# Kernel optimization log

Measured on AMD Instinct MI355X. Metric: run time of the kernel, lower is better.

## Reference

```python
import jax, jax.numpy as jnp
import numpy as np

N = 100_000        # nodes
E = 1_600_000      # edges (avg degree 16)
IN_DIM = 128
OUT_DIM = 128
EPS = 1e-5         # gnn.BatchNorm default eps


def setup_inputs() -> dict:
    key = jax.random.key(0)
    ks = jax.random.split(key, 4)
    x = jax.random.normal(ks[0], (N, IN_DIM), dtype=jnp.float32)
    edge_index = jax.random.randint(ks[1], (2, E), 0, N, dtype=jnp.int32)
    # ChebConv weights: one [indim,outdim] Linear (no bias) per hop k=0..2, plus shared bias
    W = jax.random.normal(ks[2], (3, IN_DIM, OUT_DIM), dtype=jnp.float32) / np.float32(np.sqrt(IN_DIM))
    bias = jnp.zeros((OUT_DIM,), jnp.float32)
    a_prelu = jnp.float32(0.25)           # nn.PReLU default init
    gamma = jnp.ones((OUT_DIM,), jnp.float32)
    beta = jnp.zeros((OUT_DIM,), jnp.float32)
    return dict(x=x, edge_index=edge_index, W=W, bias=bias,
                a_prelu=a_prelu, gamma=gamma, beta=beta)


def reference(x, edge_index, W, bias, a_prelu, gamma, beta):
    src, dst = edge_index[0], edge_index[1]
    n = x.shape[0]
    # --- scaled Laplacian L_hat = 2L/lambda_max - I, sym norm, lambda_max=2 ---
    # diagonal of L_hat is exactly 0 (1 from L's identity minus the -1 self-loop),
    # so only off-diagonal entries -d_i^{-1/2} d_j^{-1/2} remain.
    deg = jax.ops.segment_sum(jnp.ones_like(src, dtype=x.dtype), src, num_segments=n)
    dinv = jnp.where(deg > 0, jax.lax.rsqrt(deg), jnp.zeros_like(deg))
    norm = -(dinv[src] * dinv[dst])  # [E]

    def lhat(v):  # sparse matvec: out[i] = sum_{(j->i)} norm * v[j]
        return jax.ops.segment_sum(v[src] * norm[:, None], dst, num_segments=n)

    # --- Chebyshev recursion, K=3 ---
    tx0 = x
    tx1 = lhat(x)
    tx2 = 2.0 * lhat(tx1) - tx0
    out = tx0 @ W[0] + tx1 @ W[1] + tx2 @ W[2] + bias

    # --- PReLU (single shared parameter) ---
    out = jnp.where(out >= 0, out, a_prelu * out)

    # --- BatchNorm over nodes (training-mode batch stats, biased var) ---
    mean = out.mean(axis=0)
    var = out.var(axis=0)
    out = (out - mean) * jax.lax.rsqrt(var + EPS) * gamma + beta
    return out
```

## Files before the change

kernel.cpp:

```cpp
#include <hip/hip_runtime.h>
#include <cstdint>
#include <cstddef>

#define EPS 1e-5f
#define CAP 64
#define CHUNK 4096
#define NBMAX 256

typedef __attribute__((ext_vector_type(8))) short short8;
typedef __attribute__((ext_vector_type(4))) float f32x4;

static __device__ __forceinline__ short f2bf(float f) {
    uint32_t u = __float_as_uint(f);
    u += 0x7FFFu + ((u >> 16) & 1u);
    return (short)(u >> 16);
}
static __device__ __forceinline__ float bf2f(short s) {
    return __uint_as_float(((uint32_t)(uint16_t)s) << 16);
}

__global__ __launch_bounds__(256) void k_prep(
        const int* __restrict__ src, const int* __restrict__ dst, int E,
        const float* __restrict__ x, const float* __restrict__ W,
        int* __restrict__ bcur, int2* __restrict__ breg,
        int* __restrict__ sbcur, int* __restrict__ sbreg,
        int REGCAP, int NBK, short* __restrict__ xbf, short* __restrict__ WT,
        int BB, int SB, int TB, int t8) {
    int b = blockIdx.x;
    int t = threadIdx.x;
    __shared__ int hist[NBMAX], sexc[NBMAX], cur[NBMAX], gb[NBMAX];
    __shared__ int wsum[4];
    __shared__ int2 stage[CHUNK];
    if (b < BB) {
        int e0 = b * CHUNK;
        int2 ed[16];
        #pragma unroll
        for (int k = 0; k < 16; ++k) {
            int i = e0 + k * 256 + t;
            ed[k].x = (i < E) ? src[i] : 0;
            ed[k].y = (i < E) ? dst[i] : -1;
        }
        hist[t] = 0;
        __syncthreads();
        #pragma unroll
        for (int k = 0; k < 16; ++k)
            if (ed[k].y >= 0) atomicAdd(&hist[ed[k].y >> 9], 1);
        __syncthreads();
        int lane = t & 63, wv = t >> 6;
        int val = hist[t];
        int incl = val;
        #pragma unroll
        for (int off = 1; off < 64; off <<= 1) {
            int v = __shfl_up(incl, off);
            if (lane >= off) incl += v;
        }
        if (lane == 63) wsum[wv] = incl;
        __syncthreads();
        int bw = 0;
        for (int r = 0; r < wv; ++r) bw += wsum[r];
        int excl = bw + incl - val;
        sexc[t] = excl;
        cur[t] = excl;
        gb[t] = (val > 0 && t < NBK) ? atomicAdd(&bcur[t], val) : 0;
        __syncthreads();
        #pragma unroll
        for (int k = 0; k < 16; ++k) {
            if (ed[k].y >= 0) {
                int p = atomicAdd(&cur[ed[k].y >> 9], 1);
                stage[p] = ed[k];
            }
        }
        __syncthreads();
        int C = E - e0; if (C > CHUNK) C = CHUNK;
        for (int idx = t; idx < C; idx += 256) {
            int2 e = stage[idx];
            int bb = e.y >> 9;
            int pos = gb[bb] + (idx - sexc[bb]);
            if (pos < REGCAP) breg[(size_t)bb * REGCAP + pos] = e;
        }
    } else if (b < BB + SB) {
        int* sstage = (int*)stage;
        int e0 = (b - BB) * CHUNK;
        int es[16];
        #pragma unroll
        for (int k = 0; k < 16; ++k) {
            int i = e0 + k * 256 + t;
            es[k] = (i < E) ? src[i] : -1;
        }
        hist[t] = 0;
        __syncthreads();
        #pragma unroll
        for (int k = 0; k < 16; ++k)
            if (es[k] >= 0) atomicAdd(&hist[es[k] >> 9], 1);
        __syncthreads();
        int lane = t & 63, wv = t >> 6;
        int val = hist[t];
        int incl = val;
        #pragma unroll
        for (int off = 1; off < 64; off <<= 1) {
            int v = __shfl_up(incl, off);
            if (lane >= off) incl += v;
        }
        if (lane == 63) wsum[wv] = incl;
        __syncthreads();
        int bw = 0;
        for (int r = 0; r < wv; ++r) bw += wsum[r];
        int excl = bw + incl - val;
        sexc[t] = excl;
        cur[t] = excl;
        gb[t] = (val > 0 && t < NBK) ? atomicAdd(&sbcur[t], val) : 0;
        __syncthreads();
        #pragma unroll
        for (int k = 0; k < 16; ++k) {
            if (es[k] >= 0) {
                int p = atomicAdd(&cur[es[k] >> 9], 1);
                sstage[p] = es[k];
            }
        }
        __syncthreads();
        int C = E - e0; if (C > CHUNK) C = CHUNK;
        for (int idx = t; idx < C; idx += 256) {
            int s = sstage[idx];
            int bb = s >> 9;
            int pos = gb[bb] + (idx - sexc[bb]);
            if (pos < REGCAP) sbreg[(size_t)bb * REGCAP + pos] = s;
        }
    } else if (b < BB + SB + TB) {
        int i = (b - BB - SB) * 256 + t;
        if (i < t8) {
            const float4* s = (const float4*)x + (size_t)i * 2;
            float4 a = s[0], bb4 = s[1];
            short8 o;
            o[0] = f2bf(a.x); o[1] = f2bf(a.y); o[2] = f2bf(a.z); o[3] = f2bf(a.w);
            o[4] = f2bf(bb4.x); o[5] = f2bf(bb4.y); o[6] = f2bf(bb4.z); o[7] = f2bf(bb4.w);
            ((short8*)xbf)[i] = o;
        }
    } else {
        int i = (b - BB - SB - TB) * 256 + t;
        if (i < 16384) {
            int k = i >> 7, c = i & 127;
            float w0 = W[i], w1 = W[16384 + i], w2 = W[32768 + i];
            WT[(size_t)c * 384 + k]       = f2bf(w0 - w2);
            WT[(size_t)c * 384 + 128 + k] = f2bf(w1);
            WT[(size_t)c * 384 + 256 + k] = f2bf(2.f * w2);
        }
    }
}

__global__ __launch_bounds__(256) void k_csr(
        const int2* __restrict__ breg, const int* __restrict__ bcur,
        const int* __restrict__ sbreg, const int* __restrict__ sbcur,
        int REGCAP, int n,
        int* __restrict__ slots, int* __restrict__ cnt, float* __restrict__ dinv) {
    int b = blockIdx.x, t = threadIdx.x;
    __shared__ int c512[512], d512[512];
    c512[t] = 0; c512[t + 256] = 0;
    d512[t] = 0; d512[t + 256] = 0;
    __syncthreads();
    int M2 = sbcur[b]; if (M2 > REGCAP) M2 = REGCAP;
    const int* sreg = sbreg + (size_t)b * REGCAP;
    for (int idx = t; idx < M2; idx += 256)
        atomicAdd(&d512[sreg[idx] & 511], 1);
    int M = bcur[b]; if (M > REGCAP) M = REGCAP;
    const int2* reg = breg + (size_t)b * REGCAP;
    for (int idx = t; idx < M; idx += 256) {
        int2 e = reg[idx];
        int p = atomicAdd(&c512[e.y & 511], 1);
        if (p < CAP) slots[(size_t)e.y * CAP + p] = e.x;
    }
    __syncthreads();
    #pragma unroll
    for (int i = t; i < 512; i += 256) {
        int node = (b << 9) + i;
        if (node < n) {
            int c = c512[i];
            cnt[node] = c > CAP ? CAP : c;
            float dd = (float)d512[i];
            dinv[node] = dd > 0.f ? rsqrtf(dd) : 0.f;
        }
    }
}

__global__ void k_gather_slots(const short* __restrict__ vbf, const int* __restrict__ cnt,
                               const int* __restrict__ slots, const float* __restrict__ dinv,
                               short* __restrict__ outp, int n) {
    int row = blockIdx.x * 4 + (threadIdx.x >> 6);
    if (row >= n) return;
    int lane = threadIdx.x & 63;
    int gr = lane >> 4, lc = lane & 15;
    int deg = cnt[row];
    bool vl = lane < deg;
    int   sl = vl ? slots[(size_t)row * CAP + lane] : 0;
    float wv = vl ? dinv[sl] : 0.f;
    float acc[8];
    #pragma unroll
    for (int t = 0; t < 8; ++t) acc[t] = 0.f;
    for (int j = 0; j < deg; j += 16) {
        int j0 = j + gr;
        int   s0 = __shfl(sl, j0),      s1 = __shfl(sl, j0 + 4);
        int   s2 = __shfl(sl, j0 + 8),  s3 = __shfl(sl, j0 + 12);
        float w0 = __shfl(wv, j0),      w1 = __shfl(wv, j0 + 4);
        float w2 = __shfl(wv, j0 + 8),  w3 = __shfl(wv, j0 + 12);
        short8 xv0 = *(const short8*)(vbf + (size_t)s0 * 128 + lc * 8);
        short8 xv1 = *(const short8*)(vbf + (size_t)s1 * 128 + lc * 8);
        short8 xv2 = *(const short8*)(vbf + (size_t)s2 * 128 + lc * 8);
        short8 xv3 = *(const short8*)(vbf + (size_t)s3 * 128 + lc * 8);
        #pragma unroll
        for (int t = 0; t < 8; ++t) {
            acc[t] = fmaf(w0, bf2f(xv0[t]), acc[t]);
            acc[t] = fmaf(w1, bf2f(xv1[t]), acc[t]);
            acc[t] = fmaf(w2, bf2f(xv2[t]), acc[t]);
            acc[t] = fmaf(w3, bf2f(xv3[t]), acc[t]);
        }
    }
    #pragma unroll
    for (int t = 0; t < 8; ++t) {
        acc[t] += __shfl_xor(acc[t], 32);
        acc[t] += __shfl_xor(acc[t], 16);
    }
    if (gr == 0) {
        float sc = -dinv[row];
        short8 o;
        #pragma unroll
        for (int t = 0; t < 8; ++t) o[t] = f2bf(sc * acc[t]);
        *(short8*)(outp + (size_t)row * 128 + lc * 8) = o;
    }
}

__global__ __launch_bounds__(256) void k_gemm_mfma(
        const short* __restrict__ A0bf, const short* __restrict__ A1bf,
        const short* __restrict__ A2bf,
        const short* __restrict__ WT, const float* __restrict__ bias,
        const float* __restrict__ aprelu, float* __restrict__ out,
        float* __restrict__ partials, int NB, int n) {
    __shared__ __align__(16) short Alds[64 * 64];
    __shared__ __align__(16) short Blds[128 * 64];

    int t = threadIdx.x;
    int lane = t & 63;
    int w = t >> 6;
    int wr = w >> 1, wc = w & 1;
    int row0 = blockIdx.x * 64;

    f32x4 acc[2][4];
    #pragma unroll
    for (int m = 0; m < 2; ++m)
        #pragma unroll
        for (int nn = 0; nn < 4; ++nn) acc[m][nn] = (f32x4){0.f, 0.f, 0.f, 0.f};

    #pragma unroll
    for (int ht = 0; ht < 6; ++ht) {
        const int h = ht >> 1, c = ht & 1;
        const short* Abf = (h == 0) ? A0bf : (h == 1) ? A1bf : A2bf;

        if (ht) __syncthreads();

        #pragma unroll
        for (int i = 0; i < 4; ++i) {
            int rB = w * 32 + i * 8 + (lane >> 3);
            int blkB = (lane & 7) ^ (rB & 7);
            const short* srcB = WT + (size_t)rB * 384 + h * 128 + c * 64 + blkB * 8;
            __builtin_amdgcn_global_load_lds(
                (const __attribute__((address_space(1))) void*)srcB,
                (__attribute__((address_space(3))) void*)&Blds[(w * 32 + i * 8) * 64],
                16, 0, 0);
        }
        #pragma unroll
        for (int i = 0; i < 2; ++i) {
            int rA = w * 16 + i * 8 + (lane >> 3);
            int grow = row0 + rA; if (grow >= n) grow = n - 1;
            int blkA = (lane & 7) ^ (rA & 7);
            const short* srcA = Abf + (size_t)grow * 128 + c * 64 + blkA * 8;
            __builtin_amdgcn_global_load_lds(
                (const __attribute__((address_space(1))) void*)srcA,
                (__attribute__((address_space(3))) void*)&Alds[(w * 16 + i * 8) * 64],
                16, 0, 0);
        }
        __syncthreads();

        #pragma unroll
        for (int kk = 0; kk < 2; ++kk) {
            short8 af[2], bfr[4];
            #pragma unroll
            for (int m = 0; m < 2; ++m) {
                int row = wr * 32 + m * 16 + (lane & 15);
                int blk = (kk * 4 + (lane >> 4)) ^ (row & 7);
                af[m] = *(const short8*)((const char*)Alds + row * 128 + blk * 16);
            }
            #pragma unroll
            for (int nn = 0; nn < 4; ++nn) {
                int col = wc * 64 + nn * 16 + (lane & 15);
                int blk = (kk * 4 + (lane >> 4)) ^ (col & 7);
                bfr[nn] = *(const short8*)((const char*)Blds + col * 128 + blk * 16);
            }
            #pragma unroll
            for (int m = 0; m < 2; ++m)
                #pragma unroll
                for (int nn = 0; nn < 4; ++nn)
                    acc[m][nn] = __builtin_amdgcn_mfma_f32_16x16x32_bf16(
                        af[m], bfr[nn], acc[m][nn], 0, 0, 0);
        }
    }

    __syncthreads();
    float* sred = (float*)Alds;
    sred[t < 256 ? t : 0] = 0.f;
    __syncthreads();

    float ap = aprelu[0];
    #pragma unroll
    for (int nn = 0; nn < 4; ++nn) {
        int col = wc * 64 + nn * 16 + (lane & 15);
        float bs = bias[col];
        float s = 0.f, q = 0.f;
        #pragma unroll
        for (int m = 0; m < 2; ++m) {
            int rbase = row0 + wr * 32 + m * 16 + (lane >> 4) * 4;
            #pragma unroll
            for (int r = 0; r < 4; ++r) {
                int row = rbase + r;
                if (row < n) {
                    float o = acc[m][nn][r] + bs;
                    o = o >= 0.f ? o : ap * o;
                    out[(size_t)row * 128 + col] = o;
                    s += o; q = fmaf(o, o, q);
                }
            }
        }
        s += __shfl_xor(s, 16); s += __shfl_xor(s, 32);
        q += __shfl_xor(q, 16); q += __shfl_xor(q, 32);
        if ((lane >> 4) == 0) {
            atomicAdd(&sred[col], s);
            atomicAdd(&sred[128 + col], q);
        }
    }
    __syncthreads();
    if (t < 256) partials[(size_t)t * NB + blockIdx.x] = sred[t];
}

__global__ __launch_bounds__(256) void k_redstats(
        const float* __restrict__ partials, int NB,
        float* __restrict__ sums, float* __restrict__ sumsq) {
    int j = blockIdx.x, t = threadIdx.x;
    const float* p = partials + (size_t)j * NB;
    float s = 0.f;
    for (int i = t; i < NB; i += 256) s += p[i];
    s += __shfl_xor(s, 1); s += __shfl_xor(s, 2); s += __shfl_xor(s, 4);
    s += __shfl_xor(s, 8); s += __shfl_xor(s, 16); s += __shfl_xor(s, 32);
    __shared__ float wsum[4];
    if ((t & 63) == 0) wsum[t >> 6] = s;
    __syncthreads();
    if (t == 0) {
        float tot = wsum[0] + wsum[1] + wsum[2] + wsum[3];
        if (j < 128) sums[j] = tot;
        else sumsq[j - 128] = tot;
    }
}

__global__ void k_bnfinal(const float* __restrict__ sums, const float* __restrict__ sumsq,
                          const float* __restrict__ gamma, const float* __restrict__ beta,
                          float* __restrict__ bnp, float n) {
    int c = threadIdx.x;
    float mean = sums[c] / n;
    float var = sumsq[c] / n - mean * mean;
    float sc = gamma[c] * rsqrtf(var + EPS);
    bnp[c] = sc;
    bnp[128 + c] = beta[c] - mean * sc;
}

__global__ void k_bnapply(float* __restrict__ out, const float* __restrict__ bnp, int total4) {
    int i = blockIdx.x * blockDim.x + threadIdx.x;
    if (i >= total4) return;
    float4 v = ((float4*)out)[i];
    int c = (i * 4) & 127;
    float4 sc = *(const float4*)&bnp[c];
    float4 sh = *(const float4*)&bnp[128 + c];
    v.x = fmaf(v.x, sc.x, sh.x);
    v.y = fmaf(v.y, sc.y, sh.y);
    v.z = fmaf(v.z, sc.z, sh.z);
    v.w = fmaf(v.w, sc.w, sh.w);
    ((float4*)out)[i] = v;
}

extern "C" void kernel_launch(void* const* d_in, const int* in_sizes, int n_in,
                              void* d_out, int out_size, void* d_ws, size_t ws_size,
                              hipStream_t stream) {
    const float* x      = (const float*)d_in[0];
    const int*   ei     = (const int*)d_in[1];
    const float* W      = (const float*)d_in[2];
    const float* bias   = (const float*)d_in[3];
    const float* aprelu = (const float*)d_in[4];
    const float* gamma  = (const float*)d_in[5];
    const float* beta   = (const float*)d_in[6];
    int n = in_sizes[0] / 128;
    int E = in_sizes[1] / 2;
    const int* srcp = ei;
    const int* dstp = ei + E;

    int NBK = (n + 511) >> 9;
    int REGCAP = ((E / NBK) * 2 + 255) & ~255;
    int mb = (n + 63) / 64;

    char* ws = (char*)d_ws;
    size_t off = 0;
    auto carve = [&](size_t bytes) {
        char* p = ws + off;
        off = (off + bytes + 511) & ~(size_t)511;
        return p;
    };
    short* xbf   = (short*)carve((size_t)n * 128 * 2);
    short* tx1bf = (short*)carve((size_t)n * 128 * 2);
    int*   sbreg = (int*)tx1bf;
    size_t bregsz = (size_t)NBK * REGCAP * 8;
    size_t tx2sz  = (size_t)n * 128 * 2;
    char*  bregp  = carve(bregsz > tx2sz ? bregsz : tx2sz);
    int2*  breg   = (int2*)bregp;
    short* tx2bf  = (short*)bregp;
    size_t zbeg = off;
    int*   bcur  = (int*)carve(NBMAX * 4);
    int*   sbcur = (int*)carve(NBMAX * 4);
    size_t zend = off;
    float* sums  = (float*)carve(512);
    float* sumsq = (float*)carve(512);
    float* dinv  = (float*)carve((size_t)n * 4);
    int*   cnt   = (int*)carve((size_t)n * 4);
    int*   slots = (int*)carve((size_t)n * CAP * 4);
    short* WT    = (short*)carve((size_t)128 * 384 * 2);
    float* bnp   = (float*)carve(256 * 4);
    float* partials = (float*)carve((size_t)256 * mb * 4);
    (void)ws_size; (void)n_in; (void)out_size;

    hipMemsetAsync(ws + zbeg, 0, zend - zbeg, stream);

    int BB = (E + CHUNK - 1) / CHUNK;
    int SB = BB;
    int t8 = n * 16;
    int TB = (t8 + 255) / 256;
    k_prep<<<BB + SB + TB + 64, 256, 0, stream>>>(srcp, dstp, E, x, W, bcur, breg,
                                                  sbcur, sbreg, REGCAP, NBK, xbf, WT,
                                                  BB, SB, TB, t8);
    k_csr<<<NBK, 256, 0, stream>>>(breg, bcur, sbreg, sbcur, REGCAP, n, slots, cnt, dinv);
    int gb = (n + 3) / 4;
    k_gather_slots<<<gb, 256, 0, stream>>>(xbf, cnt, slots, dinv, tx1bf, n);
    k_gather_slots<<<gb, 256, 0, stream>>>(tx1bf, cnt, slots, dinv, tx2bf, n);
    k_gemm_mfma<<<mb, 256, 0, stream>>>(xbf, tx1bf, tx2bf, WT, bias, aprelu, (float*)d_out,
                                        partials, mb, n);
    k_redstats<<<256, 256, 0, stream>>>(partials, mb, sums, sumsq);
    k_bnfinal<<<1, 128, 0, stream>>>(sums, sumsq, gamma, beta, bnp, (float)n);
    int total4 = n * 32;
    k_bnapply<<<(total4 + 255) / 256, 256, 0, stream>>>((float*)d_out, bnp, total4);
}
```

Before: 234.6 us.

## Fuse second Laplacian gather into MFMA GEMM via LDS-resident Tx2 tile

The second sparse gather, which builds Tx2 from Tx1, now runs inside the GEMM kernel. Each block computes its 64 rows of Tx2 into a swizzled LDS tile, so the full Tx2 array is never written to or read back from global memory. The GEMM loop is also restructured to prefetch the next A/B stage right after each MFMA step. The gather inner loop is narrowed to two neighbours per step with unroll 2. The cost is more LDS per block and fewer independent waves doing the latency-bound gather, each handling 16 rows in sequence, which could reduce occupancy and latency hiding.

```diff
diff --git a/kernel.cpp b/kernel.cpp
--- a/kernel.cpp
+++ b/kernel.cpp
@@ -195,22 +195,17 @@
     float acc[8];
     #pragma unroll
     for (int t = 0; t < 8; ++t) acc[t] = 0.f;
-    for (int j = 0; j < deg; j += 16) {
-        int j0 = j + gr;
-        int   s0 = __shfl(sl, j0),      s1 = __shfl(sl, j0 + 4);
-        int   s2 = __shfl(sl, j0 + 8),  s3 = __shfl(sl, j0 + 12);
-        float w0 = __shfl(wv, j0),      w1 = __shfl(wv, j0 + 4);
-        float w2 = __shfl(wv, j0 + 8),  w3 = __shfl(wv, j0 + 12);
+    #pragma unroll 2
+    for (int j = 0; j < deg; j += 8) {
+        int j0 = j + gr, j1 = j + gr + 4;
+        int   s0 = __shfl(sl, j0), s1 = __shfl(sl, j1);
+        float w0 = __shfl(wv, j0), w1 = __shfl(wv, j1);
         short8 xv0 = *(const short8*)(vbf + (size_t)s0 * 128 + lc * 8);
         short8 xv1 = *(const short8*)(vbf + (size_t)s1 * 128 + lc * 8);
-        short8 xv2 = *(const short8*)(vbf + (size_t)s2 * 128 + lc * 8);
-        short8 xv3 = *(const short8*)(vbf + (size_t)s3 * 128 + lc * 8);
         #pragma unroll
         for (int t = 0; t < 8; ++t) {
             acc[t] = fmaf(w0, bf2f(xv0[t]), acc[t]);
             acc[t] = fmaf(w1, bf2f(xv1[t]), acc[t]);
-            acc[t] = fmaf(w2, bf2f(xv2[t]), acc[t]);
-            acc[t] = fmaf(w3, bf2f(xv3[t]), acc[t]);
         }
     }
     #pragma unroll
@@ -229,12 +224,14 @@
 
 __global__ __launch_bounds__(256) void k_gemm_mfma(
         const short* __restrict__ A0bf, const short* __restrict__ A1bf,
-        const short* __restrict__ A2bf,
         const short* __restrict__ WT, const float* __restrict__ bias,
-        const float* __restrict__ aprelu, float* __restrict__ out,
-        float* __restrict__ partials, int NB, int n) {
+        const float* __restrict__ aprelu,
+        const int* __restrict__ cnt, const int* __restrict__ slots,
+        const float* __restrict__ dinv,
+        float* __restrict__ out, float* __restrict__ partials, int NB, int n) {
     __shared__ __align__(16) short Alds[64 * 64];
     __shared__ __align__(16) short Blds[128 * 64];
+    __shared__ __align__(16) short T2[64 * 128];
 
     int t = threadIdx.x;
     int lane = t & 63;
@@ -242,19 +239,7 @@
     int wr = w >> 1, wc = w & 1;
     int row0 = blockIdx.x * 64;
 
-    f32x4 acc[2][4];
-    #pragma unroll
-    for (int m = 0; m < 2; ++m)
-        #pragma unroll
-        for (int nn = 0; nn < 4; ++nn) acc[m][nn] = (f32x4){0.f, 0.f, 0.f, 0.f};
-
-    #pragma unroll
-    for (int ht = 0; ht < 6; ++ht) {
-        const int h = ht >> 1, c = ht & 1;
-        const short* Abf = (h == 0) ? A0bf : (h == 1) ? A1bf : A2bf;
-
-        if (ht) __syncthreads();
-
+    auto stageB = [&](int h, int c) {
         #pragma unroll
         for (int i = 0; i < 4; ++i) {
             int rB = w * 32 + i * 8 + (lane >> 3);
@@ -265,6 +250,8 @@
                 (__attribute__((address_space(3))) void*)&Blds[(w * 32 + i * 8) * 64],
                 16, 0, 0);
         }
+    };
+    auto stageA = [&](const short* Abf, int c) {
         #pragma unroll
         for (int i = 0; i < 2; ++i) {
             int rA = w * 16 + i * 8 + (lane >> 3);
@@ -276,6 +263,62 @@
                 (__attribute__((address_space(3))) void*)&Alds[(w * 16 + i * 8) * 64],
                 16, 0, 0);
         }
+    };
+
+    stageB(0, 0);
+    stageA(A0bf, 0);
+
+    {
+        int gr = lane >> 4, lc = lane & 15;
+        for (int i = 0; i < 16; ++i) {
+            int r = w * 16 + i;
+            int grow = row0 + r;
+            float av[8];
+            #pragma unroll
+            for (int q = 0; q < 8; ++q) av[q] = 0.f;
+            if (grow < n) {
+                int deg = cnt[grow];
+                bool vl = lane < deg;
+                int   sl = vl ? slots[(size_t)grow * CAP + lane] : 0;
+                float wv = vl ? dinv[sl] : 0.f;
+                for (int j = 0; j < deg; j += 8) {
+                    int j0 = j + gr, j1 = j + gr + 4;
+                    int   s0 = __shfl(sl, j0), s1 = __shfl(sl, j1);
+                    float w0 = __shfl(wv, j0), w1 = __shfl(wv, j1);
+                    short8 xv0 = *(const short8*)(A1bf + (size_t)s0 * 128 + lc * 8);
+                    short8 xv1 = *(const short8*)(A1bf + (size_t)s1 * 128 + lc * 8);
+                    #pragma unroll
+                    for (int q = 0; q < 8; ++q) {
+                        av[q] = fmaf(w0, bf2f(xv0[q]), av[q]);
+                        av[q] = fmaf(w1, bf2f(xv1[q]), av[q]);
+                    }
+                }
+                #pragma unroll
+                for (int q = 0; q < 8; ++q) {
+                    av[q] += __shfl_xor(av[q], 32);
+                    av[q] += __shfl_xor(av[q], 16);
+                }
+            }
+            if (gr == 0) {
+                float sc = (grow < n) ? -dinv[grow] : 0.f;
+                short8 o;
+                #pragma unroll
+                for (int q = 0; q < 8; ++q) o[q] = f2bf(sc * av[q]);
+                int chunk = lc ^ (r & 7);
+                *(short8*)((char*)T2 + r * 256 + chunk * 16) = o;
+            }
+        }
+    }
+
+    f32x4 acc[2][4];
+    #pragma unroll
+    for (int m = 0; m < 2; ++m)
+        #pragma unroll
+        for (int nn = 0; nn < 4; ++nn) acc[m][nn] = (f32x4){0.f, 0.f, 0.f, 0.f};
+
+    #pragma unroll
+    for (int ht = 0; ht < 6; ++ht) {
+        const int h = ht >> 1, c = ht & 1;
         __syncthreads();
 
         #pragma unroll
@@ -284,8 +327,14 @@
             #pragma unroll
             for (int m = 0; m < 2; ++m) {
                 int row = wr * 32 + m * 16 + (lane & 15);
-                int blk = (kk * 4 + (lane >> 4)) ^ (row & 7);
-                af[m] = *(const short8*)((const char*)Alds + row * 128 + blk * 16);
+                int jl = kk * 4 + (lane >> 4);
+                if (h < 2) {
+                    int blk = jl ^ (row & 7);
+                    af[m] = *(const short8*)((const char*)Alds + row * 128 + blk * 16);
+                } else {
+                    int chunk = c * 8 + (jl ^ (row & 7));
+                    af[m] = *(const short8*)((const char*)T2 + row * 256 + chunk * 16);
+                }
             }
             #pragma unroll
             for (int nn = 0; nn < 4; ++nn) {
@@ -299,6 +348,13 @@
                 for (int nn = 0; nn < 4; ++nn)
                     acc[m][nn] = __builtin_amdgcn_mfma_f32_16x16x32_bf16(
                         af[m], bfr[nn], acc[m][nn], 0, 0, 0);
+        }
+
+        if (ht < 5) {
+            __syncthreads();
+            const int hn = (ht + 1) >> 1, cn = (ht + 1) & 1;
+            stageB(hn, cn);
+            if (hn < 2) stageA(hn == 0 ? A0bf : A1bf, cn);
         }
     }
 
@@ -411,11 +467,7 @@
     short* xbf   = (short*)carve((size_t)n * 128 * 2);
     short* tx1bf = (short*)carve((size_t)n * 128 * 2);
     int*   sbreg = (int*)tx1bf;
-    size_t bregsz = (size_t)NBK * REGCAP * 8;
-    size_t tx2sz  = (size_t)n * 128 * 2;
-    char*  bregp  = carve(bregsz > tx2sz ? bregsz : tx2sz);
-    int2*  breg   = (int2*)bregp;
-    short* tx2bf  = (short*)bregp;
+    int2*  breg  = (int2*)carve((size_t)NBK * REGCAP * 8);
     size_t zbeg = off;
     int*   bcur  = (int*)carve(NBMAX * 4);
     int*   sbcur = (int*)carve(NBMAX * 4);
@@ -442,9 +494,8 @@
     k_csr<<<NBK, 256, 0, stream>>>(breg, bcur, sbreg, sbcur, REGCAP, n, slots, cnt, dinv);
     int gb = (n + 3) / 4;
     k_gather_slots<<<gb, 256, 0, stream>>>(xbf, cnt, slots, dinv, tx1bf, n);
-    k_gather_slots<<<gb, 256, 0, stream>>>(tx1bf, cnt, slots, dinv, tx2bf, n);
-    k_gemm_mfma<<<mb, 256, 0, stream>>>(xbf, tx1bf, tx2bf, WT, bias, aprelu, (float*)d_out,
-                                        partials, mb, n);
+    k_gemm_mfma<<<mb, 256, 0, stream>>>(xbf, tx1bf, WT, bias, aprelu, cnt, slots, dinv,
+                                        (float*)d_out, partials, mb, n);
     k_redstats<<<256, 256, 0, stream>>>(partials, mb, sums, sumsq);
     k_bnfinal<<<1, 128, 0, stream>>>(sums, sumsq, gamma, beta, bnp, (float)n);
     int total4 = n * 32;
```

Measured after the change: 257.1 us. +9.6%, slower.

## Load GEMM weight fragments directly from global and shrink gather unroll width

Applied to the files above, without the earlier changes.

The GEMM kernel no longer stages the weight tile in LDS. Each wave reads its B fragments straight from global memory, relying on cache hits because the 96KB bf16 weight is shared by all blocks. This removes the LDS allocation and the async copy traffic, which may raise occupancy, but the global loads are less coalesced and sit closer to the MFMA issue. Separately, the gather loop now handles 2 neighbors per step instead of 4, unrolled by 2, which changes register pressure and how much memory-level parallelism each iteration exposes.

```diff
diff --git a/kernel.cpp b/kernel.cpp
--- a/kernel.cpp
+++ b/kernel.cpp
@@ -195,22 +195,17 @@
     float acc[8];
     #pragma unroll
     for (int t = 0; t < 8; ++t) acc[t] = 0.f;
-    for (int j = 0; j < deg; j += 16) {
-        int j0 = j + gr;
-        int   s0 = __shfl(sl, j0),      s1 = __shfl(sl, j0 + 4);
-        int   s2 = __shfl(sl, j0 + 8),  s3 = __shfl(sl, j0 + 12);
-        float w0 = __shfl(wv, j0),      w1 = __shfl(wv, j0 + 4);
-        float w2 = __shfl(wv, j0 + 8),  w3 = __shfl(wv, j0 + 12);
+    #pragma unroll 2
+    for (int j = 0; j < deg; j += 8) {
+        int j0 = j + gr, j1 = j + gr + 4;
+        int   s0 = __shfl(sl, j0), s1 = __shfl(sl, j1);
+        float w0 = __shfl(wv, j0), w1 = __shfl(wv, j1);
         short8 xv0 = *(const short8*)(vbf + (size_t)s0 * 128 + lc * 8);
         short8 xv1 = *(const short8*)(vbf + (size_t)s1 * 128 + lc * 8);
-        short8 xv2 = *(const short8*)(vbf + (size_t)s2 * 128 + lc * 8);
-        short8 xv3 = *(const short8*)(vbf + (size_t)s3 * 128 + lc * 8);
         #pragma unroll
         for (int t = 0; t < 8; ++t) {
             acc[t] = fmaf(w0, bf2f(xv0[t]), acc[t]);
             acc[t] = fmaf(w1, bf2f(xv1[t]), acc[t]);
-            acc[t] = fmaf(w2, bf2f(xv2[t]), acc[t]);
-            acc[t] = fmaf(w3, bf2f(xv3[t]), acc[t]);
         }
     }
     #pragma unroll
@@ -234,7 +229,6 @@
         const float* __restrict__ aprelu, float* __restrict__ out,
         float* __restrict__ partials, int NB, int n) {
     __shared__ __align__(16) short Alds[64 * 64];
-    __shared__ __align__(16) short Blds[128 * 64];
 
     int t = threadIdx.x;
     int lane = t & 63;
@@ -255,16 +249,6 @@
 
         if (ht) __syncthreads();
 
-        #pragma unroll
-        for (int i = 0; i < 4; ++i) {
-            int rB = w * 32 + i * 8 + (lane >> 3);
-            int blkB = (lane & 7) ^ (rB & 7);
-            const short* srcB = WT + (size_t)rB * 384 + h * 128 + c * 64 + blkB * 8;
-            __builtin_amdgcn_global_load_lds(
-                (const __attribute__((address_space(1))) void*)srcB,
-                (__attribute__((address_space(3))) void*)&Blds[(w * 32 + i * 8) * 64],
-                16, 0, 0);
-        }
         #pragma unroll
         for (int i = 0; i < 2; ++i) {
             int rA = w * 16 + i * 8 + (lane >> 3);
@@ -280,18 +264,18 @@
 
         #pragma unroll
         for (int kk = 0; kk < 2; ++kk) {
+            int jl = kk * 4 + (lane >> 4);
             short8 af[2], bfr[4];
             #pragma unroll
             for (int m = 0; m < 2; ++m) {
                 int row = wr * 32 + m * 16 + (lane & 15);
-                int blk = (kk * 4 + (lane >> 4)) ^ (row & 7);
+                int blk = jl ^ (row & 7);
                 af[m] = *(const short8*)((const char*)Alds + row * 128 + blk * 16);
             }
             #pragma unroll
             for (int nn = 0; nn < 4; ++nn) {
                 int col = wc * 64 + nn * 16 + (lane & 15);
-                int blk = (kk * 4 + (lane >> 4)) ^ (col & 7);
-                bfr[nn] = *(const short8*)((const char*)Blds + col * 128 + blk * 16);
+                bfr[nn] = *(const short8*)(WT + (size_t)col * 384 + h * 128 + c * 64 + jl * 8);
             }
             #pragma unroll
             for (int m = 0; m < 2; ++m)
```

Result: slower. 259.3 us (+10.5%).
